# Kernel tuning notes

Measured on AMD Instinct MI355X. Metric: run time of the kernel, lower is better.

## Reference

```python
import jax, jax.numpy as jnp
import numpy as np

NUM_GROUPS = 32
EPS = 1e-6


def group_norm(x, gamma, beta):
    # x: [B, C, H, W]
    B, C, H, W = x.shape
    xg = x.reshape(B, NUM_GROUPS, C // NUM_GROUPS, H, W)
    mean = jnp.mean(xg, axis=(2, 3, 4), keepdims=True)
    var = jnp.var(xg, axis=(2, 3, 4), keepdims=True)
    xn = (xg - mean) * jax.lax.rsqrt(var + EPS)
    xn = xn.reshape(B, C, H, W)
    return xn * gamma[None, :, None, None] + beta[None, :, None, None]


def conv1x1(x, w, b):
    # x: [B, C, H, W], w: [Cout, Cin], b: [Cout]
    return jnp.einsum('bchw,dc->bdhw', x, w) + b[None, :, None, None]


def setup_inputs() -> dict:
    key = jax.random.key(0)
    ks = jax.random.split(key, 11)
    B, C, H, W = 4, 512, 64, 64
    s = 1.0 / np.sqrt(C)
    return {
        'x': jax.random.normal(ks[0], (B, C, H, W), dtype=jnp.float32),
        'gn_gamma': jnp.ones((C,), dtype=jnp.float32),
        'gn_beta': jnp.zeros((C,), dtype=jnp.float32),
        'wq': jax.random.normal(ks[1], (C, C), dtype=jnp.float32) * s,
        'bq': jax.random.normal(ks[2], (C,), dtype=jnp.float32) * 0.01,
        'wk': jax.random.normal(ks[3], (C, C), dtype=jnp.float32) * s,
        'bk': jax.random.normal(ks[4], (C,), dtype=jnp.float32) * 0.01,
        'wv': jax.random.normal(ks[5], (C, C), dtype=jnp.float32) * s,
        'bv': jax.random.normal(ks[6], (C,), dtype=jnp.float32) * 0.01,
        'wo': jax.random.normal(ks[7], (C, C), dtype=jnp.float32) * s,
        'bo': jax.random.normal(ks[8], (C,), dtype=jnp.float32) * 0.01,
    }


def reference(x, gn_gamma, gn_beta, wq, bq, wk, bk, wv, bv, wo, bo):
    B, C, H, W = x.shape
    h = group_norm(x, gn_gamma, gn_beta)
    q = conv1x1(h, wq, bq).reshape(B, C, H * W)  # [B, C, N]
    k = conv1x1(h, wk, bk).reshape(B, C, H * W)
    v = conv1x1(h, wv, bv).reshape(B, C, H * W)
    scale = jnp.asarray(C, x.dtype) ** -0.5
    # scores[b, i, j] = q_i . k_j
    scores = jnp.einsum('bci,bcj->bij', q, k) * scale  # [B, N, N]
    attn = jax.nn.softmax(scores, axis=2)
    # out[b, c, i] = sum_j v[b, c, j] * attn[b, i, j]
    out = jnp.einsum('bcj,bij->bci', v, attn).reshape(B, C, H, W)
    out = conv1x1(out, wo, bo)
    return x + out
```

## Files before the change

kernel.cpp:

```cpp
#include <hip/hip_runtime.h>

using uint = unsigned int;
typedef short bf16x8 __attribute__((ext_vector_type(8)));
typedef _Float16 f16x8 __attribute__((ext_vector_type(8)));
typedef float f32x4 __attribute__((ext_vector_type(4)));
typedef long i64;
typedef i64 i64x2 __attribute__((ext_vector_type(2)));
typedef i64 i64x4 __attribute__((ext_vector_type(4)));
typedef int i32x8 __attribute__((ext_vector_type(8)));
typedef unsigned short u16x4 __attribute__((ext_vector_type(4)));

static constexpr int Cc = 512;
static constexpr int Nn = 4096;
static constexpr size_t NC = (size_t)Nn * Cc;
static constexpr size_t SN = (size_t)Nn * Nn;

__device__ __forceinline__ unsigned short f2bf(float f) {
    unsigned int u = __builtin_bit_cast(unsigned int, f);
    u = (u + 0x7fff + ((u >> 16) & 1)) >> 16;
    return (unsigned short)u;
}
__device__ __forceinline__ unsigned short f2h(float f) {
    _Float16 h = (_Float16)f;
    return __builtin_bit_cast(unsigned short, h);
}

__device__ __forceinline__ void gll16(const void* g, void* l) {
    __builtin_amdgcn_global_load_lds(
        (const __attribute__((address_space(1))) void*)g,
        (__attribute__((address_space(3))) void*)l, 16, 0, 0);
}

__device__ __forceinline__ f32x4 mfma_fp8_k128(i32x8 a, i32x8 b, f32x4 c) {
    return __builtin_amdgcn_mfma_scale_f32_16x16x128_f8f6f4(
        a, b, c, 0 , 0 , 0, 0x7F7F7F7F, 0, 0x7F7F7F7F);
}

__device__ __forceinline__ i32x8 ld_frag256(const unsigned char* base, int R, int g0) {
    const unsigned char* p = base + R * 128;
    i64x2 l0 = *(const i64x2*)(p + ((g0 ^ (R & 7)) << 4));
    i64x2 l1 = *(const i64x2*)(p + (((g0 + 1) ^ (R & 7)) << 4));
    i64x4 c4 = {l0[0], l0[1], l1[0], l1[1]};
    return __builtin_bit_cast(i32x8, c4);
}

__global__ void cvt_kernel(const float* __restrict__ in, unsigned short* __restrict__ out, int n4) {
    int i = blockIdx.x * blockDim.x + threadIdx.x;
    if (i < n4) {
        float4 v = ((const float4*)in)[i];
        out[i * 4 + 0] = f2bf(v.x);
        out[i * 4 + 1] = f2bf(v.y);
        out[i * 4 + 2] = f2bf(v.z);
        out[i * 4 + 3] = f2bf(v.w);
    }
}

__global__ void zero_kernel(float* __restrict__ p, int n4) {
    int i = blockIdx.x * blockDim.x + threadIdx.x;
    if (i < n4) ((float4*)p)[i] = make_float4(0.f, 0.f, 0.f, 0.f);
}

__global__ void gn_stats_kernel(const float* __restrict__ x, float* __restrict__ meanb,
                                float* __restrict__ rsb) {
    int bg = blockIdx.x;
    const float* slab = x + (size_t)bg * 16 * Nn;
    const float4* s4 = (const float4*)slab;
    int t = threadIdx.x;
    float s1 = 0.f, s2 = 0.f;
#pragma unroll 8
    for (int k = 0; k < 64; ++k) {
        float4 v = s4[k * 256 + t];
        s1 += v.x + v.y + v.z + v.w;
        s2 += v.x * v.x + v.y * v.y + v.z * v.z + v.w * v.w;
    }
#pragma unroll
    for (int o = 32; o > 0; o >>= 1) { s1 += __shfl_down(s1, o); s2 += __shfl_down(s2, o); }
    __shared__ float r1[4], r2[4];
    int wv_ = t >> 6, ln = t & 63;
    if (ln == 0) { r1[wv_] = s1; r2[wv_] = s2; }
    __syncthreads();
    if (t == 0) {
        float a1 = r1[0] + r1[1] + r1[2] + r1[3];
        float a2 = r2[0] + r2[1] + r2[2] + r2[3];
        float mean = a1 * (1.f / 65536.f);
        float var = a2 * (1.f / 65536.f) - mean * mean;
        meanb[bg] = mean;
        rsb[bg] = rsqrtf(var + 1e-6f);
    }
}

__global__ __launch_bounds__(256) void gn_norm_kernel(
    const float* __restrict__ x, const float* __restrict__ meanb, const float* __restrict__ rsb,
    const float* __restrict__ gamma, const float* __restrict__ beta,
    unsigned short* __restrict__ h_t) {
    __shared__ float tile[64][65];
    int n0 = blockIdx.x * 64, c0 = blockIdx.y * 64, b = blockIdx.z;
    int t = threadIdx.x;
    const float* xb = x + (size_t)b * Cc * Nn;
#pragma unroll
    for (int j = 0; j < 4; ++j) {
        int i = j * 256 + t;
        int c = i >> 4;
        int n4 = i & 15;
        int cg = c0 + c;
        float4 v = ((const float4*)(xb + (size_t)cg * Nn + n0))[n4];
        int g = cg >> 4;
        float mean = meanb[b * 32 + g], rs = rsb[b * 32 + g];
        float ga = gamma[cg] * rs;
        float be = beta[cg] - mean * ga;
        tile[n4 * 4 + 0][c] = v.x * ga + be;
        tile[n4 * 4 + 1][c] = v.y * ga + be;
        tile[n4 * 4 + 2][c] = v.z * ga + be;
        tile[n4 * 4 + 3][c] = v.w * ga + be;
    }
    __syncthreads();
    int n = t >> 2;
    int cpart = (t & 3) * 16;
    unsigned short o[16];
#pragma unroll
    for (int q = 0; q < 16; ++q) o[q] = f2bf(tile[n][cpart + q]);
    unsigned short* dst = h_t + (size_t)b * NC + (size_t)(n0 + n) * Cc + c0 + cpart;
    ((uint4*)dst)[0] = ((uint4*)o)[0];
    ((uint4*)dst)[1] = ((uint4*)o)[1];
}

template <int BM, int DT, int BIAS_MODE, int OUT_MODE, int HAS_RES>
__global__ __launch_bounds__(256, 2) void gemm_bt(
    const unsigned short* __restrict__ A, int lda, size_t sA,
    const unsigned short* __restrict__ Bt, int ldb, size_t sB,
    void* __restrict__ outp, int ldc, size_t sC,
    const float* __restrict__ bias,
    const float* __restrict__ res, size_t sR,
    int K, float alpha) {
    constexpr int MT = BM / 32;
    __shared__ unsigned short lA[BM * 64];
    __shared__ unsigned short lB[128 * 64];
    int z = blockIdx.z;
    A += (size_t)z * sA;
    Bt += (size_t)z * sB;
    int m0 = blockIdx.y * BM, n0 = blockIdx.x * 128;
    int t = threadIdx.x;
    int lane = t & 63, wave = t >> 6;
    int wm = wave >> 1, wn = wave & 1;
    int lo = lane & 15, quad = lane >> 4;

    f32x4 acc[MT][4];
#pragma unroll
    for (int a1 = 0; a1 < MT; ++a1)
#pragma unroll
        for (int a2 = 0; a2 < 4; ++a2) acc[a1][a2] = (f32x4){0.f, 0.f, 0.f, 0.f};

    for (int k0 = 0; k0 < K; k0 += 64) {
#pragma unroll
        for (int p = 0; p < MT; ++p) {
            int ci = p * 256 + t;
            int row = ci >> 3;
            int gs = (ci ^ row) & 7;
            gll16(A + (size_t)(m0 + row) * lda + k0 + gs * 8, &lA[(size_t)ci * 8]);
        }
#pragma unroll
        for (int p = 0; p < 4; ++p) {
            int ci = p * 256 + t;
            int row = ci >> 3;
            int gs = (ci ^ row) & 7;
            gll16(Bt + (size_t)(n0 + row) * ldb + k0 + gs * 8, &lB[(size_t)ci * 8]);
        }
        __syncthreads();
#pragma unroll
        for (int ks = 0; ks < 2; ++ks) {
            int G = quad + ks * 4;
            bf16x8 af[MT], bfr[4];
#pragma unroll
            for (int mt = 0; mt < MT; ++mt) {
                int R = wm * (BM / 2) + mt * 16 + lo;
                af[mt] = *(const bf16x8*)&lA[R * 64 + (((G ^ R) & 7) << 3)];
            }
#pragma unroll
            for (int nt = 0; nt < 4; ++nt) {
                int R = wn * 64 + nt * 16 + lo;
                bfr[nt] = *(const bf16x8*)&lB[R * 64 + (((G ^ R) & 7) << 3)];
            }
#pragma unroll
            for (int mt = 0; mt < MT; ++mt)
#pragma unroll
                for (int nt = 0; nt < 4; ++nt) {
                    if (DT == 0)
                        acc[mt][nt] = __builtin_amdgcn_mfma_f32_16x16x32_bf16(af[mt], bfr[nt], acc[mt][nt], 0, 0, 0);
                    else
                        acc[mt][nt] = __builtin_amdgcn_mfma_f32_16x16x32_f16(
                            __builtin_bit_cast(f16x8, af[mt]), __builtin_bit_cast(f16x8, bfr[nt]),
                            acc[mt][nt], 0, 0, 0);
                }
        }
        __syncthreads();
    }

    size_t zc = (size_t)z * sC;
    float* outf = (float*)outp + zc;
    unsigned short* outb = (unsigned short*)outp + zc;
    unsigned char* outc = (unsigned char*)outp + zc;
    const float* resz = HAS_RES ? res + (size_t)z * sR : nullptr;

#pragma unroll
    for (int mt = 0; mt < MT; ++mt) {
#pragma unroll
        for (int nt = 0; nt < 4; ++nt) {
            int row = m0 + wm * (BM / 2) + mt * 16 + quad * 4;
            int col = n0 + wn * 64 + nt * 16 + lo;
            float bn = (BIAS_MODE == 2) ? bias[col] : 0.f;
#pragma unroll
            for (int r = 0; r < 4; ++r) {
                float vv = acc[mt][nt][r];
                if (BIAS_MODE == 1) vv += bias[row + r];
                if (BIAS_MODE == 2) vv += bn;
                vv *= alpha;
                if (OUT_MODE == 3) {
                    float e = fmaxf(fminf(vv, 448.f), -448.f);
                    int pk = __builtin_amdgcn_cvt_pk_fp8_f32(e, e, 0, false);
                    outc[(size_t)(row + r) * ldc + col] = (unsigned char)(pk & 0xff);
                } else {
                    size_t off = (size_t)(row + r) * ldc + col;
                    if (HAS_RES) vv += resz[off];
                    if (OUT_MODE == 0) outf[off] = vv;
                    else if (OUT_MODE == 1) outb[off] = f2bf(vv);
                    else outb[off] = f2h(vv);
                }
            }
        }
    }
}

__global__ __launch_bounds__(256, 3) void qk_fp8(
    const unsigned char* __restrict__ Q, const unsigned char* __restrict__ Kt,
    unsigned char* __restrict__ S, float* __restrict__ lsum, float alpha) {
    __shared__ unsigned char lA[128 * 128];
    __shared__ unsigned char lB[128 * 128];
    int z = blockIdx.z;
    Q += (size_t)z * NC;
    Kt += (size_t)z * NC;
    S += (size_t)z * SN;
    lsum += (size_t)z * Nn;
    int m0 = blockIdx.y * 128, n0 = blockIdx.x * 128;
    int t = threadIdx.x;
    int lane = t & 63, wave = t >> 6;
    int wm = wave >> 1, wn = wave & 1;
    int lo = lane & 15, quad = lane >> 4;

    f32x4 acc[4][4];
#pragma unroll
    for (int a1 = 0; a1 < 4; ++a1)
#pragma unroll
        for (int a2 = 0; a2 < 4; ++a2) acc[a1][a2] = (f32x4){0.f, 0.f, 0.f, 0.f};

    for (int k0 = 0; k0 < Cc; k0 += 128) {
#pragma unroll
        for (int p = 0; p < 4; ++p) {
            int ci = p * 256 + t;
            int row = ci >> 3, g = ci & 7;
            int gs = g ^ (row & 7);
            gll16(Q + (size_t)(m0 + row) * Cc + k0 + gs * 16, &lA[ci * 16]);
        }
#pragma unroll
        for (int p = 0; p < 4; ++p) {
            int ci = p * 256 + t;
            int row = ci >> 3, g = ci & 7;
            int gs = g ^ (row & 7);
            gll16(Kt + (size_t)(n0 + row) * Cc + k0 + gs * 16, &lB[ci * 16]);
        }
        __syncthreads();
        int g0 = quad * 2;
        i32x8 qf[4];
#pragma unroll
        for (int qt = 0; qt < 4; ++qt) qf[qt] = ld_frag256(lA, wm * 64 + qt * 16 + lo, g0);
#pragma unroll
        for (int jt = 0; jt < 4; ++jt) {
            i32x8 kf = ld_frag256(lB, wn * 64 + jt * 16 + lo, g0);
#pragma unroll
            for (int qt = 0; qt < 4; ++qt)
                acc[jt][qt] = mfma_fp8_k128(kf, qf[qt], acc[jt][qt]);
        }
        __syncthreads();
    }

    float rs[4] = {0.f, 0.f, 0.f, 0.f};
#pragma unroll
    for (int jt = 0; jt < 4; ++jt) {
        int j = n0 + wn * 64 + jt * 16 + quad * 4;
#pragma unroll
        for (int qt = 0; qt < 4; ++qt) {
            int q = m0 + wm * 64 + qt * 16 + lo;
            float e0 = fminf(__expf(acc[jt][qt][0] * alpha - 2.f), 448.f);
            float e1 = fminf(__expf(acc[jt][qt][1] * alpha - 2.f), 448.f);
            float e2 = fminf(__expf(acc[jt][qt][2] * alpha - 2.f), 448.f);
            float e3 = fminf(__expf(acc[jt][qt][3] * alpha - 2.f), 448.f);
            int d = __builtin_amdgcn_cvt_pk_fp8_f32(e0, e1, 0, false);
            d = __builtin_amdgcn_cvt_pk_fp8_f32(e2, e3, d, true);
            *(uint*)&S[(size_t)q * Nn + j] = (uint)d;
            rs[qt] += __builtin_amdgcn_cvt_f32_fp8(d, 0) + __builtin_amdgcn_cvt_f32_fp8(d, 1) +
                      __builtin_amdgcn_cvt_f32_fp8(d, 2) + __builtin_amdgcn_cvt_f32_fp8(d, 3);
        }
    }
#pragma unroll
    for (int qt = 0; qt < 4; ++qt) {
        rs[qt] += __shfl_xor(rs[qt], 16);
        rs[qt] += __shfl_xor(rs[qt], 32);
    }
    if (quad == 0) {
#pragma unroll
        for (int qt = 0; qt < 4; ++qt)
            atomicAdd(&lsum[m0 + wm * 64 + qt * 16 + lo], rs[qt]);
    }
}

__global__ __launch_bounds__(256, 3) void pv_fp8(
    const unsigned char* __restrict__ S, const unsigned char* __restrict__ V,
    const float* __restrict__ lsum, unsigned short* __restrict__ o_t) {
    __shared__ unsigned char lA[128 * 128];
    __shared__ unsigned char lB[128 * 128];
    int z = blockIdx.z;
    S += (size_t)z * SN;
    V += (size_t)z * NC;
    lsum += (size_t)z * Nn;
    o_t += (size_t)z * NC;
    int m0 = blockIdx.y * 128, n0 = blockIdx.x * 128;
    int t = threadIdx.x;
    int lane = t & 63, wave = t >> 6;
    int wm = wave >> 1, wn = wave & 1;
    int lo = lane & 15, quad = lane >> 4;

    f32x4 acc[4][4];
#pragma unroll
    for (int a1 = 0; a1 < 4; ++a1)
#pragma unroll
        for (int a2 = 0; a2 < 4; ++a2) acc[a1][a2] = (f32x4){0.f, 0.f, 0.f, 0.f};

    for (int k0 = 0; k0 < Nn; k0 += 128) {
#pragma unroll
        for (int p = 0; p < 4; ++p) {
            int ci = p * 256 + t;
            int row = ci >> 3, g = ci & 7;
            int gs = g ^ (row & 7);
            gll16(S + (size_t)(m0 + row) * Nn + k0 + gs * 16, &lA[ci * 16]);
        }
#pragma unroll
        for (int p = 0; p < 4; ++p) {
            int ci = p * 256 + t;
            int row = ci >> 3, g = ci & 7;
            int gs = g ^ (row & 7);
            gll16(V + (size_t)(n0 + row) * Nn + k0 + gs * 16, &lB[ci * 16]);
        }
        __syncthreads();
        int g0 = quad * 2;
        i32x8 sf[4];
#pragma unroll
        for (int qt = 0; qt < 4; ++qt) sf[qt] = ld_frag256(lA, wm * 64 + qt * 16 + lo, g0);
#pragma unroll
        for (int ct = 0; ct < 4; ++ct) {
            i32x8 vf = ld_frag256(lB, wn * 64 + ct * 16 + lo, g0);
#pragma unroll
            for (int qt = 0; qt < 4; ++qt)
                acc[ct][qt] = mfma_fp8_k128(vf, sf[qt], acc[ct][qt]);
        }
        __syncthreads();
    }

#pragma unroll
    for (int qt = 0; qt < 4; ++qt) {
        int q = m0 + wm * 64 + qt * 16 + lo;
        float inv = 1.f / lsum[q];
#pragma unroll
        for (int ct = 0; ct < 4; ++ct) {
            int c = n0 + wn * 64 + ct * 16 + quad * 4;
            u16x4 o;
            o[0] = f2bf(acc[ct][qt][0] * inv);
            o[1] = f2bf(acc[ct][qt][1] * inv);
            o[2] = f2bf(acc[ct][qt][2] * inv);
            o[3] = f2bf(acc[ct][qt][3] * inv);
            *(u16x4*)&o_t[(size_t)q * Cc + c] = o;
        }
    }
}

extern "C" void kernel_launch(void* const* d_in, const int* in_sizes, int n_in,
                              void* d_out, int out_size, void* d_ws, size_t ws_size,
                              hipStream_t stream) {
    const float* x     = (const float*)d_in[0];
    const float* gamma = (const float*)d_in[1];
    const float* beta  = (const float*)d_in[2];
    const float* wq = (const float*)d_in[3];
    const float* bq = (const float*)d_in[4];
    const float* wk = (const float*)d_in[5];
    const float* bk = (const float*)d_in[6];
    const float* wv = (const float*)d_in[7];
    const float* bv = (const float*)d_in[8];
    const float* wo = (const float*)d_in[9];
    const float* bo = (const float*)d_in[10];

    char* ws = (char*)d_ws;
    unsigned short* h_t  = (unsigned short*)(ws);
    unsigned char*  q_8  = (unsigned char*)(ws + 16777216);
    unsigned char*  k_8  = (unsigned char*)(ws + 33554432);
    unsigned char*  v_8  = (unsigned char*)(ws + 50331648);
    unsigned short* o_t  = (unsigned short*)(ws + 67108864);
    unsigned char*  S    = (unsigned char*)(ws + 83886080);
    unsigned short* wqb  = (unsigned short*)(ws + 218103808);
    unsigned short* wkb  = (unsigned short*)(ws + 218628096);
    unsigned short* wvb  = (unsigned short*)(ws + 219152384);
    unsigned short* wob  = (unsigned short*)(ws + 219676672);
    float* statm         = (float*)(ws + 220200960);
    float* statr         = (float*)(ws + 220201984);
    float* lsum          = (float*)(ws + 220203008);

    const float SCALE = 0.044194173824159216f;

    cvt_kernel<<<256, 256, 0, stream>>>(wq, wqb, 65536);
    cvt_kernel<<<256, 256, 0, stream>>>(wk, wkb, 65536);
    cvt_kernel<<<256, 256, 0, stream>>>(wv, wvb, 65536);
    cvt_kernel<<<256, 256, 0, stream>>>(wo, wob, 65536);
    zero_kernel<<<16, 256, 0, stream>>>(lsum, 4096);

    gn_stats_kernel<<<128, 256, 0, stream>>>(x, statm, statr);
    gn_norm_kernel<<<dim3(64, 8, 4), 256, 0, stream>>>(x, statm, statr, gamma, beta, h_t);

    gemm_bt<128, 0, 2, 3, 0><<<dim3(4, 32, 4), 256, 0, stream>>>(
        h_t, Cc, NC, wqb, Cc, 0, q_8, Cc, NC, bq, nullptr, 0, Cc, 1.f);
    gemm_bt<128, 0, 2, 3, 0><<<dim3(4, 32, 4), 256, 0, stream>>>(
        h_t, Cc, NC, wkb, Cc, 0, k_8, Cc, NC, bk, nullptr, 0, Cc, 1.f);
    gemm_bt<128, 0, 1, 3, 0><<<dim3(32, 4, 4), 256, 0, stream>>>(
        wvb, Cc, 0, h_t, Cc, NC, v_8, Nn, NC, bv, nullptr, 0, Cc, 1.f);

    qk_fp8<<<dim3(32, 32, 4), 256, 0, stream>>>(q_8, k_8, S, lsum, SCALE);
    pv_fp8<<<dim3(4, 32, 4), 256, 0, stream>>>(S, v_8, lsum, o_t);

    gemm_bt<128, 0, 1, 0, 1><<<dim3(32, 4, 4), 256, 0, stream>>>(
        wob, Cc, 0, o_t, Cc, NC, d_out, Nn, NC, bo, x, NC, Cc, 1.f);
}
```

Measured before the change: 302.6 us.

## Fuse weight conversions and Q/K projections, compute softmax row sums inside PV via MFMA

The four weight-conversion launches merge into one kernel, the lsum zeroing launch is dropped, and the Q and K projections run as a single GEMM launch that routes column blocks past 512 to the K output. The softmax row-sum atomics in qk_fp8 are removed. pv_fp8 now computes the row sums itself with an extra fp8 MFMA against a ones vector (0x38 is fp8 1.0). qk_fp8 also gets a remapped block order for locality and a launch bound of 4 blocks per CU. These changes cut launch overhead and atomic traffic, at the cost of extra MFMA work in pv_fp8 and more register pressure in qk_fp8.

```diff
diff --git a/kernel.cpp b/kernel.cpp
--- a/kernel.cpp
+++ b/kernel.cpp
@@ -44,20 +44,18 @@
     return __builtin_bit_cast(i32x8, c4);
 }
 
-__global__ void cvt_kernel(const float* __restrict__ in, unsigned short* __restrict__ out, int n4) {
+__global__ void cvt4_kernel(const float* __restrict__ wa, const float* __restrict__ wb,
+                            const float* __restrict__ wc, const float* __restrict__ wd,
+                            unsigned short* __restrict__ out) {
+    const float* ins[4] = {wa, wb, wc, wd};
+    const float* in = ins[blockIdx.y];
+    unsigned short* o = out + (size_t)blockIdx.y * 262144;
     int i = blockIdx.x * blockDim.x + threadIdx.x;
-    if (i < n4) {
-        float4 v = ((const float4*)in)[i];
-        out[i * 4 + 0] = f2bf(v.x);
-        out[i * 4 + 1] = f2bf(v.y);
-        out[i * 4 + 2] = f2bf(v.z);
-        out[i * 4 + 3] = f2bf(v.w);
-    }
-}
-
-__global__ void zero_kernel(float* __restrict__ p, int n4) {
-    int i = blockIdx.x * blockDim.x + threadIdx.x;
-    if (i < n4) ((float4*)p)[i] = make_float4(0.f, 0.f, 0.f, 0.f);
+    float4 v = ((const float4*)in)[i];
+    o[i * 4 + 0] = f2bf(v.x);
+    o[i * 4 + 1] = f2bf(v.y);
+    o[i * 4 + 2] = f2bf(v.z);
+    o[i * 4 + 3] = f2bf(v.w);
 }
 
 __global__ void gn_stats_kernel(const float* __restrict__ x, float* __restrict__ meanb,
@@ -131,7 +129,8 @@
     void* __restrict__ outp, int ldc, size_t sC,
     const float* __restrict__ bias,
     const float* __restrict__ res, size_t sR,
-    int K, float alpha) {
+    int K, float alpha,
+    const float* __restrict__ bias2, void* __restrict__ outp2, int nsplit) {
     constexpr int MT = BM / 32;
     __shared__ unsigned short lA[BM * 64];
     __shared__ unsigned short lB[128 * 64];
@@ -139,6 +138,8 @@
     A += (size_t)z * sA;
     Bt += (size_t)z * sB;
     int m0 = blockIdx.y * BM, n0 = blockIdx.x * 128;
+    int ncol0 = n0;
+    if (nsplit && n0 >= nsplit) { bias = bias2; outp = outp2; ncol0 = n0 - nsplit; }
     int t = threadIdx.x;
     int lane = t & 63, wave = t >> 6;
     int wm = wave >> 1, wn = wave & 1;
@@ -206,7 +207,7 @@
 #pragma unroll
         for (int nt = 0; nt < 4; ++nt) {
             int row = m0 + wm * (BM / 2) + mt * 16 + quad * 4;
-            int col = n0 + wn * 64 + nt * 16 + lo;
+            int col = ncol0 + wn * 64 + nt * 16 + lo;
             float bn = (BIAS_MODE == 2) ? bias[col] : 0.f;
 #pragma unroll
             for (int r = 0; r < 4; ++r) {
@@ -230,17 +231,19 @@
     }
 }
 
-__global__ __launch_bounds__(256, 3) void qk_fp8(
+__global__ __launch_bounds__(256, 4) void qk_fp8(
     const unsigned char* __restrict__ Q, const unsigned char* __restrict__ Kt,
-    unsigned char* __restrict__ S, float* __restrict__ lsum, float alpha) {
+    unsigned char* __restrict__ S, float alpha) {
     __shared__ unsigned char lA[128 * 128];
     __shared__ unsigned char lB[128 * 128];
-    int z = blockIdx.z;
+    int flat = blockIdx.x + (blockIdx.y << 5) + (blockIdx.z << 10);
+    int nid = ((flat & 7) << 9) + (flat >> 3);
+    int bx = nid & 31, by = (nid >> 5) & 31, bz = nid >> 10;
+    int z = bz;
     Q += (size_t)z * NC;
     Kt += (size_t)z * NC;
     S += (size_t)z * SN;
-    lsum += (size_t)z * Nn;
-    int m0 = blockIdx.y * 128, n0 = blockIdx.x * 128;
+    int m0 = by * 128, n0 = bx * 128;
     int t = threadIdx.x;
     int lane = t & 63, wave = t >> 6;
     int wm = wave >> 1, wn = wave & 1;
@@ -282,7 +285,6 @@
         __syncthreads();
     }
 
-    float rs[4] = {0.f, 0.f, 0.f, 0.f};
 #pragma unroll
     for (int jt = 0; jt < 4; ++jt) {
         int j = n0 + wn * 64 + jt * 16 + quad * 4;
@@ -296,31 +298,18 @@
             int d = __builtin_amdgcn_cvt_pk_fp8_f32(e0, e1, 0, false);
             d = __builtin_amdgcn_cvt_pk_fp8_f32(e2, e3, d, true);
             *(uint*)&S[(size_t)q * Nn + j] = (uint)d;
-            rs[qt] += __builtin_amdgcn_cvt_f32_fp8(d, 0) + __builtin_amdgcn_cvt_f32_fp8(d, 1) +
-                      __builtin_amdgcn_cvt_f32_fp8(d, 2) + __builtin_amdgcn_cvt_f32_fp8(d, 3);
-        }
-    }
-#pragma unroll
-    for (int qt = 0; qt < 4; ++qt) {
-        rs[qt] += __shfl_xor(rs[qt], 16);
-        rs[qt] += __shfl_xor(rs[qt], 32);
-    }
-    if (quad == 0) {
-#pragma unroll
-        for (int qt = 0; qt < 4; ++qt)
-            atomicAdd(&lsum[m0 + wm * 64 + qt * 16 + lo], rs[qt]);
+        }
     }
 }
 
 __global__ __launch_bounds__(256, 3) void pv_fp8(
     const unsigned char* __restrict__ S, const unsigned char* __restrict__ V,
-    const float* __restrict__ lsum, unsigned short* __restrict__ o_t) {
+    unsigned short* __restrict__ o_t) {
     __shared__ unsigned char lA[128 * 128];
     __shared__ unsigned char lB[128 * 128];
     int z = blockIdx.z;
     S += (size_t)z * SN;
     V += (size_t)z * NC;
-    lsum += (size_t)z * Nn;
     o_t += (size_t)z * NC;
     int m0 = blockIdx.y * 128, n0 = blockIdx.x * 128;
     int t = threadIdx.x;
@@ -329,10 +318,15 @@
     int lo = lane & 15, quad = lane >> 4;
 
     f32x4 acc[4][4];
-#pragma unroll
-    for (int a1 = 0; a1 < 4; ++a1)
+    f32x4 rs[4];
+#pragma unroll
+    for (int a1 = 0; a1 < 4; ++a1) {
+        rs[a1] = (f32x4){0.f, 0.f, 0.f, 0.f};
 #pragma unroll
         for (int a2 = 0; a2 < 4; ++a2) acc[a1][a2] = (f32x4){0.f, 0.f, 0.f, 0.f};
+    }
+    const int OB = 0x38383838;
+    const i32x8 ones = {OB, OB, OB, OB, OB, OB, OB, OB};
 
     for (int k0 = 0; k0 < Nn; k0 += 128) {
 #pragma unroll
@@ -353,7 +347,10 @@
         int g0 = quad * 2;
         i32x8 sf[4];
 #pragma unroll
-        for (int qt = 0; qt < 4; ++qt) sf[qt] = ld_frag256(lA, wm * 64 + qt * 16 + lo, g0);
+        for (int qt = 0; qt < 4; ++qt) {
+            sf[qt] = ld_frag256(lA, wm * 64 + qt * 16 + lo, g0);
+            rs[qt] = mfma_fp8_k128(ones, sf[qt], rs[qt]);
+        }
 #pragma unroll
         for (int ct = 0; ct < 4; ++ct) {
             i32x8 vf = ld_frag256(lB, wn * 64 + ct * 16 + lo, g0);
@@ -367,7 +364,7 @@
 #pragma unroll
     for (int qt = 0; qt < 4; ++qt) {
         int q = m0 + wm * 64 + qt * 16 + lo;
-        float inv = 1.f / lsum[q];
+        float inv = 1.f / rs[qt][0];
 #pragma unroll
         for (int ct = 0; ct < 4; ++ct) {
             int c = n0 + wn * 64 + ct * 16 + quad * 4;
@@ -404,34 +401,26 @@
     unsigned short* o_t  = (unsigned short*)(ws + 67108864);
     unsigned char*  S    = (unsigned char*)(ws + 83886080);
     unsigned short* wqb  = (unsigned short*)(ws + 218103808);
-    unsigned short* wkb  = (unsigned short*)(ws + 218628096);
     unsigned short* wvb  = (unsigned short*)(ws + 219152384);
     unsigned short* wob  = (unsigned short*)(ws + 219676672);
     float* statm         = (float*)(ws + 220200960);
     float* statr         = (float*)(ws + 220201984);
-    float* lsum          = (float*)(ws + 220203008);
 
     const float SCALE = 0.044194173824159216f;
 
-    cvt_kernel<<<256, 256, 0, stream>>>(wq, wqb, 65536);
-    cvt_kernel<<<256, 256, 0, stream>>>(wk, wkb, 65536);
-    cvt_kernel<<<256, 256, 0, stream>>>(wv, wvb, 65536);
-    cvt_kernel<<<256, 256, 0, stream>>>(wo, wob, 65536);
-    zero_kernel<<<16, 256, 0, stream>>>(lsum, 4096);
+    cvt4_kernel<<<dim3(256, 4), 256, 0, stream>>>(wq, wk, wv, wo, wqb);
 
     gn_stats_kernel<<<128, 256, 0, stream>>>(x, statm, statr);
     gn_norm_kernel<<<dim3(64, 8, 4), 256, 0, stream>>>(x, statm, statr, gamma, beta, h_t);
 
-    gemm_bt<128, 0, 2, 3, 0><<<dim3(4, 32, 4), 256, 0, stream>>>(
-        h_t, Cc, NC, wqb, Cc, 0, q_8, Cc, NC, bq, nullptr, 0, Cc, 1.f);
-    gemm_bt<128, 0, 2, 3, 0><<<dim3(4, 32, 4), 256, 0, stream>>>(
-        h_t, Cc, NC, wkb, Cc, 0, k_8, Cc, NC, bk, nullptr, 0, Cc, 1.f);
+    gemm_bt<128, 0, 2, 3, 0><<<dim3(8, 32, 4), 256, 0, stream>>>(
+        h_t, Cc, NC, wqb, Cc, 0, q_8, Cc, NC, bq, nullptr, 0, Cc, 1.f, bk, k_8, 512);
     gemm_bt<128, 0, 1, 3, 0><<<dim3(32, 4, 4), 256, 0, stream>>>(
-        wvb, Cc, 0, h_t, Cc, NC, v_8, Nn, NC, bv, nullptr, 0, Cc, 1.f);
-
-    qk_fp8<<<dim3(32, 32, 4), 256, 0, stream>>>(q_8, k_8, S, lsum, SCALE);
-    pv_fp8<<<dim3(4, 32, 4), 256, 0, stream>>>(S, v_8, lsum, o_t);
+        wvb, Cc, 0, h_t, Cc, NC, v_8, Nn, NC, bv, nullptr, 0, Cc, 1.f, nullptr, nullptr, 0);
+
+    qk_fp8<<<dim3(32, 32, 4), 256, 0, stream>>>(q_8, k_8, S, SCALE);
+    pv_fp8<<<dim3(4, 32, 4), 256, 0, stream>>>(S, v_8, o_t);
 
     gemm_bt<128, 0, 1, 0, 1><<<dim3(32, 4, 4), 256, 0, stream>>>(
-        wob, Cc, 0, o_t, Cc, NC, d_out, Nn, NC, bo, x, NC, Cc, 1.f);
-}
+        wob, Cc, 0, o_t, Cc, NC, d_out, Nn, NC, bo, x, NC, Cc, 1.f, nullptr, nullptr, 0);
+}
```

Result: no change. 304.9 us (+0.7%).
